# Kernel optimization log

Hardware: AMD Instinct MI355X
Metric: run time of the kernel (lower is better)

The kernel has to match this reference:

```python
import jax, jax.numpy as jnp
import numpy as np

ATTEN_SIZE = 5  # half-window; module-global atten_size in source (0 there is non-functional)
B, S, D_IN, HID, OUT = 8, 2048, 512, 512, 2


def _xavier(key, shape):
    fan_in, fan_out = shape
    std = (2.0 / (fan_in + fan_out)) ** 0.5
    return jax.random.normal(key, shape, dtype=jnp.float32) * std


def setup_inputs() -> dict:
    key = jax.random.key(0)
    ks = jax.random.split(key, 8)
    return {
        "x": jax.random.normal(ks[0], (B, S, D_IN), dtype=jnp.float32),
        "W1": _xavier(ks[1], (D_IN, HID)),
        "b1": jnp.zeros((1, 1, HID), dtype=jnp.float32),
        "Wq": _xavier(ks[2], (HID, HID)),
        "Wk": _xavier(ks[3], (HID, HID)),
        "Wv": _xavier(ks[4], (HID, HID)),
        "W2": _xavier(ks[5], (HID, HID)),
        "b2": jnp.zeros((1, 1, HID), dtype=jnp.float32),
        "Wfc": _xavier(ks[6], (HID, OUT)),
        "bfc": jnp.zeros((OUT,), dtype=jnp.float32),
    }


def reference(x, W1, b1, Wq, Wk, Wv, W2, b2, Wfc, bfc):
    A = ATTEN_SIZE
    Wn = 2 * A + 1
    h = jax.nn.relu(x @ W1 + b1)                      # [B,S,H]
    b, s, hd = h.shape
    padded = jnp.pad(h, ((0, 0), (A, A), (0, 0)))     # [B,S+2A,H]
    # torch pad+roll(k)+stack+slice equals reversed window: x_nei[p, j] = padded[p + 2A - j]
    idx = jnp.arange(s)[:, None] + (2 * A - jnp.arange(Wn))[None, :]  # [S,Wn]
    x_nei = padded[:, idx, :]                         # [B,S,Wn,H]
    q = h @ Wq                                        # [B,S,H]
    k = x_nei @ Wk                                    # [B,S,Wn,H]
    v = x_nei @ Wv                                    # [B,S,Wn,H]
    scale = jnp.asarray(np.sqrt(float(hd)), dtype=h.dtype)
    scores = jnp.einsum('bsh,bswh->bsw', q, k)[:, :, None, :] / scale  # [B,S,1,Wn]
    # Faithful to torch.nn.Softmax(dim=2) on a singleton dim -> all ones
    w = jax.nn.softmax(scores, axis=2)                # [B,S,1,Wn]
    aw = jnp.einsum('bsjw,bswh->bsjh', w, v).reshape(b, s, hd)  # [B,S,H]
    out = jax.nn.relu(aw @ W2 + b2) @ Wfc + bfc       # [B,S,OUT]
    return out, aw
```

## Files before the change

### kernel.cpp

```cpp
#include <hip/hip_runtime.h>
#include <stdint.h>

#define B_   8
#define S_   2048
#define HID_ 512
#define M_   (B_ * S_)
#define AW_  5

typedef __attribute__((ext_vector_type(8))) short bf16x8;
typedef __attribute__((ext_vector_type(4))) float f32x4;
typedef unsigned short u16;

__device__ __forceinline__ u16 f2bf(float f) {
    uint32_t u = __builtin_bit_cast(uint32_t, f);
    u += 0x7FFFu + ((u >> 16) & 1u);
    return (u16)(u >> 16);
}
__device__ __forceinline__ float bf2f(u16 h) {
    uint32_t u = ((uint32_t)h) << 16;
    return __builtin_bit_cast(float, u);
}

__device__ __forceinline__ void gload16(const void* g, void* l) {
    __builtin_amdgcn_global_load_lds(
        (const __attribute__((address_space(1))) void*)(uintptr_t)g,
        (__attribute__((address_space(3))) void*)(uint32_t)(uintptr_t)l,
        16, 0, 0);
}

#define WAITV(n)  asm volatile("s_waitcnt vmcnt(" #n ")" ::: "memory")
#define WAITLG0() asm volatile("s_waitcnt lgkmcnt(0)" ::: "memory")

__global__ __launch_bounds__(256) void prep_w(const float* __restrict__ W1,
                                              const float* __restrict__ Wv,
                                              const float* __restrict__ W2,
                                              u16* __restrict__ W1t,
                                              u16* __restrict__ Wvt,
                                              u16* __restrict__ W2t,
                                              int do_w2) {
    const int wsel = blockIdx.x >> 8;
    if (wsel == 2 && !do_w2) return;
    const float* src = wsel == 0 ? W1 : (wsel == 1 ? Wv : W2);
    u16* dst = wsel == 0 ? W1t : (wsel == 1 ? Wvt : W2t);
    const int t  = blockIdx.x & 255;
    const int n0 = (t & 15) * 32, k0 = (t >> 4) * 32;
    __shared__ float tile[32][33];
    const int tr = threadIdx.x >> 5, tc = threadIdx.x & 31;
#pragma unroll
    for (int p = 0; p < 4; ++p)
        tile[tr + p * 8][tc] = src[(long)(k0 + tr + p * 8) * HID_ + n0 + tc];
    __syncthreads();
#pragma unroll
    for (int p = 0; p < 4; ++p)
        dst[(long)(n0 + tr + p * 8) * HID_ + k0 + tc] = f2bf(tile[tc][tr + p * 8]);
}

__global__ __launch_bounds__(256) void trans_w2(const float* __restrict__ W2,
                                                u16* __restrict__ W2t) {
    __shared__ float tile[32][33];
    const int k0 = blockIdx.y * 32, n0 = blockIdx.x * 32;
    const int tr = threadIdx.x >> 5, tc = threadIdx.x & 31;
#pragma unroll
    for (int p = 0; p < 4; ++p)
        tile[tr + p * 8][tc] = W2[(long)(k0 + tr + p * 8) * HID_ + n0 + tc];
    __syncthreads();
#pragma unroll
    for (int p = 0; p < 4; ++p)
        W2t[(long)(n0 + tr + p * 8) * HID_ + k0 + tc] = f2bf(tile[tc][tr + p * 8]);
}

__global__ __launch_bounds__(256, 2) void gemm1_f32a(const float* __restrict__ A,
                                                     const u16* __restrict__ Bt,
                                                     const float* __restrict__ bias,
                                                     u16* __restrict__ C) {
    __shared__ __attribute__((aligned(16))) u16 As[2][128 * 64];
    __shared__ __attribute__((aligned(16))) u16 Bs[2][128 * 64];

    const int tid = threadIdx.x;
    const int bid = blockIdx.x;
    const int swz = (bid & 7) * 64 + (bid >> 3);
    const int  bn   = (swz & 3) * 128;
    const long brow = (long)(swz >> 2) * 128;

    const int w  = tid >> 6;
    const int l  = tid & 63;
    const int wm = (w >> 1) * 64;
    const int wn = (w & 1) * 64;
    const int lr  = l & 15;
    const int lkb = (l >> 4) * 16;
    const int sw  = (lr & 7) << 4;

    const int r0 = tid >> 2;
    const int c0 = (tid & 3) * 16;
    const int r1 = 64 + r0;
    const float* ga0 = A + (brow + r0) * 512 + c0;
    const float* ga1 = A + (brow + r1) * 512 + c0;
    char* lw = (char*)&As[0][0];
    const int wb00 = r0 * 128 + ((c0 * 2 +  0) ^ ((r0 & 7) << 4));
    const int wb01 = r0 * 128 + ((c0 * 2 + 16) ^ ((r0 & 7) << 4));
    const int wb10 = r1 * 128 + ((c0 * 2 +  0) ^ ((r1 & 7) << 4));
    const int wb11 = r1 * 128 + ((c0 * 2 + 16) ^ ((r1 & 7) << 4));

    int pq[4];
    const u16* srcB[4];
#pragma unroll
    for (int q = 0; q < 4; ++q) {
        const int p   = tid * 16 + q * 4096;
        const int row = p >> 7;
        const int cb  = (p & 127) ^ ((row & 7) << 4);
        pq[q]   = p;
        srcB[q] = Bt + (long)(bn + row) * 512 + (cb >> 1);
    }

    f32x4 acc[4][4];
#pragma unroll
    for (int i = 0; i < 4; ++i)
#pragma unroll
        for (int j = 0; j < 4; ++j) {
            f32x4 z = {0.f, 0.f, 0.f, 0.f};
            acc[i][j] = z;
        }

    float4 ra[4], rb[4];

#define LOADA(k0)                                                        \
    {                                                                    \
        _Pragma("unroll") for (int u = 0; u < 4; ++u) {                  \
            ra[u] = *(const float4*)(ga0 + (k0) + u * 4);                \
            rb[u] = *(const float4*)(ga1 + (k0) + u * 4);                \
        }                                                                \
    }
#define CVTWRITE(buf)                                                    \
    {                                                                    \
        union { u16 u[8]; int4 v; } q0, q1, q2, q3;                      \
        q0.u[0]=f2bf(ra[0].x); q0.u[1]=f2bf(ra[0].y); q0.u[2]=f2bf(ra[0].z); q0.u[3]=f2bf(ra[0].w); \
        q0.u[4]=f2bf(ra[1].x); q0.u[5]=f2bf(ra[1].y); q0.u[6]=f2bf(ra[1].z); q0.u[7]=f2bf(ra[1].w); \
        q1.u[0]=f2bf(ra[2].x); q1.u[1]=f2bf(ra[2].y); q1.u[2]=f2bf(ra[2].z); q1.u[3]=f2bf(ra[2].w); \
        q1.u[4]=f2bf(ra[3].x); q1.u[5]=f2bf(ra[3].y); q1.u[6]=f2bf(ra[3].z); q1.u[7]=f2bf(ra[3].w); \
        q2.u[0]=f2bf(rb[0].x); q2.u[1]=f2bf(rb[0].y); q2.u[2]=f2bf(rb[0].z); q2.u[3]=f2bf(rb[0].w); \
        q2.u[4]=f2bf(rb[1].x); q2.u[5]=f2bf(rb[1].y); q2.u[6]=f2bf(rb[1].z); q2.u[7]=f2bf(rb[1].w); \
        q3.u[0]=f2bf(rb[2].x); q3.u[1]=f2bf(rb[2].y); q3.u[2]=f2bf(rb[2].z); q3.u[3]=f2bf(rb[2].w); \
        q3.u[4]=f2bf(rb[3].x); q3.u[5]=f2bf(rb[3].y); q3.u[6]=f2bf(rb[3].z); q3.u[7]=f2bf(rb[3].w); \
        *(int4*)(lw + (buf) * 16384 + wb00) = q0.v;                      \
        *(int4*)(lw + (buf) * 16384 + wb01) = q1.v;                      \
        *(int4*)(lw + (buf) * 16384 + wb10) = q2.v;                      \
        *(int4*)(lw + (buf) * 16384 + wb11) = q3.v;                      \
    }
#define STAGEB(buf, k0)                                                  \
    {                                                                    \
        _Pragma("unroll") for (int q = 0; q < 4; ++q)                    \
            gload16(srcB[q] + (k0), (char*)&Bs[buf][0] + pq[q]);         \
    }

    LOADA(0);
    STAGEB(0, 0);
    CVTWRITE(0);
    __syncthreads();

    int cur = 0;
    for (int t = 0; t < 8; ++t) {
        if (t < 7) {
            LOADA((t + 1) * 64);
            STAGEB(cur ^ 1, (t + 1) * 64);
        }
#pragma unroll
        for (int kk = 0; kk < 2; ++kk) {
            bf16x8 af[4], bfr[4];
#pragma unroll
            for (int i = 0; i < 4; ++i) {
                const int off = (wm + i * 16 + lr) * 128 + ((kk * 64 + lkb) ^ sw);
                af[i] = *(const bf16x8*)((const char*)&As[cur][0] + off);
            }
#pragma unroll
            for (int j = 0; j < 4; ++j) {
                const int off = (wn + j * 16 + lr) * 128 + ((kk * 64 + lkb) ^ sw);
                bfr[j] = *(const bf16x8*)((const char*)&Bs[cur][0] + off);
            }
#pragma unroll
            for (int i = 0; i < 4; ++i)
#pragma unroll
                for (int j = 0; j < 4; ++j)
                    acc[i][j] = __builtin_amdgcn_mfma_f32_16x16x32_bf16(
                        af[i], bfr[j], acc[i][j], 0, 0, 0);
        }
        if (t < 7) CVTWRITE(cur ^ 1);
        __syncthreads();
        cur ^= 1;
    }
#undef LOADA
#undef CVTWRITE
#undef STAGEB

    float bv[4];
#pragma unroll
    for (int j = 0; j < 4; ++j) bv[j] = bias[bn + wn + j * 16 + lr];
    const int rq = (l >> 4) * 4;
#pragma unroll
    for (int i = 0; i < 4; ++i)
#pragma unroll
        for (int q = 0; q < 4; ++q) {
            const long row = brow + wm + i * 16 + rq + q;
            u16* crow = C + row * 512 + bn + wn + lr;
#pragma unroll
            for (int j = 0; j < 4; ++j)
                crow[j * 16] = f2bf(fmaxf(acc[i][j][q] + bv[j], 0.f));
        }
}

template <int EPI>
__global__ __launch_bounds__(256, 2) void gemm128(const u16* __restrict__ A,
                                                  const u16* __restrict__ Bt,
                                                  const float* __restrict__ b2,
                                                  const float* __restrict__ Wfc,
                                                  u16* __restrict__ C,
                                                  float* __restrict__ partials) {
    __shared__ __attribute__((aligned(16))) u16 As[2][128 * 64];
    __shared__ __attribute__((aligned(16))) u16 Bs[2][128 * 64];

    const int tid = threadIdx.x;
    const int bid = blockIdx.x;
    const int swz = (bid & 7) * 64 + (bid >> 3);
    const int  bn   = (swz & 3) * 128;
    const long brow = (long)(swz >> 2) * 128;

    const int w  = tid >> 6;
    const int l  = tid & 63;
    const int wm = (w >> 1) * 64;
    const int wn = (w & 1) * 64;
    const int lr  = l & 15;
    const int lkb = (l >> 4) * 16;
    const int sw  = (lr & 7) << 4;

    int pq[4];
    const u16* srcA[4];
    const u16* srcB[4];
#pragma unroll
    for (int q = 0; q < 4; ++q) {
        const int p   = tid * 16 + q * 4096;
        const int row = p >> 7;
        const int cb  = (p & 127) ^ ((row & 7) << 4);
        pq[q]   = p;
        srcA[q] = A  + (brow + row) * 512 + (cb >> 1);
        srcB[q] = Bt + (long)(bn + row) * 512 + (cb >> 1);
    }

    f32x4 acc[4][4];
#pragma unroll
    for (int i = 0; i < 4; ++i)
#pragma unroll
        for (int j = 0; j < 4; ++j) {
            f32x4 z = {0.f, 0.f, 0.f, 0.f};
            acc[i][j] = z;
        }

#define STAGE(buf, k0)                                                   \
    {                                                                    \
        _Pragma("unroll") for (int q = 0; q < 4; ++q) {                  \
            gload16(srcA[q] + (k0), (char*)&As[buf][0] + pq[q]);         \
            gload16(srcB[q] + (k0), (char*)&Bs[buf][0] + pq[q]);         \
        }                                                                \
    }

    int cur = 0;
    STAGE(0, 0);
    __syncthreads();

    for (int t = 0; t < 8; ++t) {
        if (t < 7) STAGE(cur ^ 1, (t + 1) * 64);
#pragma unroll
        for (int kk = 0; kk < 2; ++kk) {
            bf16x8 af[4], bfr[4];
#pragma unroll
            for (int i = 0; i < 4; ++i) {
                const int off = (wm + i * 16 + lr) * 128 + ((kk * 64 + lkb) ^ sw);
                af[i] = *(const bf16x8*)((const char*)&As[cur][0] + off);
            }
#pragma unroll
            for (int j = 0; j < 4; ++j) {
                const int off = (wn + j * 16 + lr) * 128 + ((kk * 64 + lkb) ^ sw);
                bfr[j] = *(const bf16x8*)((const char*)&Bs[cur][0] + off);
            }
#pragma unroll
            for (int i = 0; i < 4; ++i)
#pragma unroll
                for (int j = 0; j < 4; ++j)
                    acc[i][j] = __builtin_amdgcn_mfma_f32_16x16x32_bf16(
                        af[i], bfr[j], acc[i][j], 0, 0, 0);
        }
        __syncthreads();
        cur ^= 1;
    }
#undef STAGE

    const int rq = (l >> 4) * 4;
    if (EPI == 0) {
#pragma unroll
        for (int i = 0; i < 4; ++i)
#pragma unroll
            for (int q = 0; q < 4; ++q) {
                const long row = brow + wm + i * 16 + rq + q;
                u16* crow = C + row * 512 + bn + wn + lr;
#pragma unroll
                for (int j = 0; j < 4; ++j)
                    crow[j * 16] = f2bf(acc[i][j][q]);
            }
    } else {
        float bvv[4], w0v[4], w1v[4];
#pragma unroll
        for (int j = 0; j < 4; ++j) {
            const int col = bn + wn + j * 16 + lr;
            bvv[j] = b2[col];
            w0v[j] = Wfc[2 * col];
            w1v[j] = Wfc[2 * col + 1];
        }
        const int slot = (bn >> 7) * 2 + (wn >> 6);
#pragma unroll
        for (int i = 0; i < 4; ++i)
#pragma unroll
            for (int q = 0; q < 4; ++q) {
                float s0 = 0.f, s1 = 0.f;
#pragma unroll
                for (int j = 0; j < 4; ++j) {
                    const float v = fmaxf(acc[i][j][q] + bvv[j], 0.f);
                    s0 += v * w0v[j];
                    s1 += v * w1v[j];
                }
#pragma unroll
                for (int m = 1; m < 16; m <<= 1) {
                    s0 += __shfl_xor(s0, m);
                    s1 += __shfl_xor(s1, m);
                }
                if (lr == 0) {
                    const long row = brow + wm + i * 16 + rq + q;
                    float* pp = partials + ((long)slot * M_ + row) * 2;
                    pp[0] = s0;
                    pp[1] = s1;
                }
            }
    }
}

__global__ __launch_bounds__(512, 2) void gemm2_ws(const u16* __restrict__ A,
                                                   const u16* __restrict__ Bt,
                                                   u16* __restrict__ awb,
                                                   float* __restrict__ awf) {
    __shared__ __attribute__((aligned(16))) u16 As[3][288 * 64];
    __shared__ __attribute__((aligned(16))) u16 Bs[3][128 * 64];

    const int tid = threadIdx.x;
    const int bid = blockIdx.x;
    const int swz = (bid & 7) * 32 + (bid >> 3);
    const int  bn   = (swz & 3) * 128;
    const long brow = (long)(swz >> 2) * 256;

    const int w  = tid >> 6;
    const int l  = tid & 63;
    const int wm = (w >> 2) * 144;
    const int wn = (w & 3) * 32;
    const int lr  = l & 15;
    const int lkb = (l >> 4) * 16;
    const int sw  = (lr & 7) << 4;
    const bool loww = (tid < 256);

    int pa[5];
    const u16* srcA[5];
#pragma unroll
    for (int q = 0; q < 4; ++q) {
        const int p   = tid * 16 + q * 8192;
        const int row = p >> 7;
        const int cb  = (p & 127) ^ ((row & 7) << 4);
        long R = brow - 16 + row;
        R = R < 0 ? 0 : (R > M_ - 1 ? M_ - 1 : R);
        pa[q]   = p;
        srcA[q] = A + R * 512 + (cb >> 1);
    }
    pa[4] = 0; srcA[4] = A;
    if (loww) {
        const int p   = 32768 + tid * 16;
        const int row = p >> 7;
        const int cb  = (p & 127) ^ ((row & 7) << 4);
        long R = brow - 16 + row;
        R = R < 0 ? 0 : (R > M_ - 1 ? M_ - 1 : R);
        pa[4]   = p;
        srcA[4] = A + R * 512 + (cb >> 1);
    }
    int pb[2];
    const u16* srcB[2];
#pragma unroll
    for (int q = 0; q < 2; ++q) {
        const int p   = tid * 16 + q * 8192;
        const int row = p >> 7;
        const int cb  = (p & 127) ^ ((row & 7) << 4);
        pb[q]   = p;
        srcB[q] = Bt + (long)(bn + row) * 512 + (cb >> 1);
    }

    f32x4 acc[9][2];
#pragma unroll
    for (int i = 0; i < 9; ++i)
#pragma unroll
        for (int j = 0; j < 2; ++j) {
            f32x4 z = {0.f, 0.f, 0.f, 0.f};
            acc[i][j] = z;
        }

#define STG(buf, k0)                                                     \
    {                                                                    \
        gload16(srcA[0] + (k0), (char*)&As[buf][0] + pa[0]);             \
        gload16(srcA[1] + (k0), (char*)&As[buf][0] + pa[1]);             \
        gload16(srcA[2] + (k0), (char*)&As[buf][0] + pa[2]);             \
        gload16(srcA[3] + (k0), (char*)&As[buf][0] + pa[3]);             \
        if (loww) gload16(srcA[4] + (k0), (char*)&As[buf][0] + pa[4]);   \
        gload16(srcB[0] + (k0), (char*)&Bs[buf][0] + pb[0]);             \
        gload16(srcB[1] + (k0), (char*)&Bs[buf][0] + pb[1]);             \
    }
#define WAITP()                                                          \
    do {                                                                 \
        if (loww) { WAITV(7); } else { WAITV(6); }                       \
    } while (0)

    STG(0, 0);
    STG(1, 64);
    WAITP();
    __builtin_amdgcn_s_barrier();

#pragma unroll
    for (int t = 0; t < 8; ++t) {
        if (t < 6) {
            const int nb = (t + 2) % 3;
            if (nb == 0)      STG(0, (t + 2) * 64)
            else if (nb == 1) STG(1, (t + 2) * 64)
            else              STG(2, (t + 2) * 64)
        }

        const int cbuf = t % 3;
        const char* ab = cbuf == 0 ? (const char*)&As[0][0]
                       : cbuf == 1 ? (const char*)&As[1][0] : (const char*)&As[2][0];
        const char* bb = cbuf == 0 ? (const char*)&Bs[0][0]
                       : cbuf == 1 ? (const char*)&Bs[1][0] : (const char*)&Bs[2][0];

        __builtin_amdgcn_s_setprio(1);
#pragma unroll
        for (int kk = 0; kk < 2; ++kk) {
            bf16x8 af[9], bfr[2];
#pragma unroll
            for (int j = 0; j < 2; ++j) {
                const int off = (wn + j * 16 + lr) * 128 + ((kk * 64 + lkb) ^ sw);
                bfr[j] = *(const bf16x8*)(bb + off);
            }
#pragma unroll
            for (int i = 0; i < 9; ++i) {
                const int off = (wm + i * 16 + lr) * 128 + ((kk * 64 + lkb) ^ sw);
                af[i] = *(const bf16x8*)(ab + off);
            }
#pragma unroll
            for (int i = 0; i < 9; ++i)
#pragma unroll
                for (int j = 0; j < 2; ++j)
                    acc[i][j] = __builtin_amdgcn_mfma_f32_16x16x32_bf16(
                        af[i], bfr[j], acc[i][j], 0, 0, 0);
        }
        __builtin_amdgcn_s_setprio(0);

        if (t < 7) {
            WAITLG0();
            __builtin_amdgcn_sched_barrier(0);
            if (t < 6) { WAITP(); } else { WAITV(0); }
            __builtin_amdgcn_s_barrier();
        }
    }
#undef STG
#undef WAITP

    __syncthreads();
    u16* gl = &As[0][0];

    const int rq4 = (l >> 4) * 4;
#pragma unroll
    for (int i = 0; i < 9; ++i)
#pragma unroll
        for (int j = 0; j < 2; ++j)
#pragma unroll
            for (int q = 0; q < 4; ++q) {
                const int row = wm + i * 16 + rq4 + q;
                const int col = wn + j * 16 + lr;
                gl[row * 128 + col] = f2bf(acc[i][j][q]);
            }
    __syncthreads();

    for (int rr = 0; rr < 32; ++rr) {
        const int  rloc = w * 32 + rr;
        const long R    = brow + rloc;
        const int  s    = (int)(R & (S_ - 1));
        float a0 = 0.f, a1 = 0.f;
#pragma unroll
        for (int d = -AW_; d <= AW_; ++d) {
            if ((unsigned)(s + d) < (unsigned)S_) {
                const uint32_t v =
                    *(const uint32_t*)&gl[(rloc + 16 + d) * 128 + 2 * l];
                a0 += bf2f((u16)(v & 0xffffu));
                a1 += bf2f((u16)(v >> 16));
            }
        }
        const uint32_t pk = (uint32_t)f2bf(a0) | ((uint32_t)f2bf(a1) << 16);
        *(uint32_t*)&awb[R * 512 + bn + 2 * l] = pk;
        float2 o; o.x = a0; o.y = a1;
        *(float2*)&awf[R * 512 + bn + 2 * l] = o;
    }
}

__global__ __launch_bounds__(256) void winsum_f(const u16* __restrict__ g,
                                                u16* __restrict__ awb,
                                                float* __restrict__ awf) {
    const long idx = (long)blockIdx.x * 256 + threadIdx.x;
    const int  c8  = (int)(idx & 63);
    const long bs  = idx >> 6;
    const int  s   = (int)(bs & (S_ - 1));

    float acc[8] = {};
#pragma unroll
    for (int d = -AW_; d <= AW_; ++d) {
        const int ss = s + d;
        if (0 <= ss && ss < S_) {
            const int4 v = *(const int4*)&g[(bs + d) * HID_ + c8 * 8];
            const u16* u = (const u16*)&v;
#pragma unroll
            for (int e = 0; e < 8; ++e) acc[e] += bf2f(u[e]);
        }
    }
    union { u16 u[8]; int4 v; } r;
#pragma unroll
    for (int e = 0; e < 8; ++e) r.u[e] = f2bf(acc[e]);
    *(int4*)&awb[bs * HID_ + c8 * 8] = r.v;
    float4 o0 = {acc[0], acc[1], acc[2], acc[3]};
    float4 o1 = {acc[4], acc[5], acc[6], acc[7]};
    *(float4*)&awf[bs * HID_ + c8 * 8]     = o0;
    *(float4*)&awf[bs * HID_ + c8 * 8 + 4] = o1;
}

__global__ __launch_bounds__(256) void fc_reduce(const float* __restrict__ partials,
                                                 const float* __restrict__ bfc,
                                                 float* __restrict__ out) {
    const int row = blockIdx.x * 256 + threadIdx.x;
    float s0 = bfc[0], s1 = bfc[1];
#pragma unroll
    for (int p = 0; p < 8; ++p) {
        s0 += partials[((long)p * M_ + row) * 2 + 0];
        s1 += partials[((long)p * M_ + row) * 2 + 1];
    }
    out[row * 2 + 0] = s0;
    out[row * 2 + 1] = s1;
}

extern "C" void kernel_launch(void* const* d_in, const int* in_sizes, int n_in,
                              void* d_out, int out_size, void* d_ws, size_t ws_size,
                              hipStream_t stream) {
    const float* x   = (const float*)d_in[0];
    const float* W1  = (const float*)d_in[1];
    const float* b1  = (const float*)d_in[2];
    const float* Wv  = (const float*)d_in[5];
    const float* W2  = (const float*)d_in[6];
    const float* b2  = (const float*)d_in[7];
    const float* Wfc = (const float*)d_in[8];
    const float* bfc = (const float*)d_in[9];

    float* out_part = (float*)d_out;
    float* aw_f32   = (float*)d_out + (long)M_ * 2;

    unsigned char* ws = (unsigned char*)d_ws;

    const bool big = ws_size >= ((size_t)35 << 20);

    if (big) {
        u16* h    = (u16*)ws;
        u16* awb  = (u16*)(ws + (16l << 20));
        u16* W1t  = (u16*)(ws + (32l << 20));
        u16* Wvt  = W1t + 262144;
        u16* W2t  = Wvt + 262144;
        float* partials = (float*)(ws + (33l << 20) + (1l << 19));

        prep_w<<<768, 256, 0, stream>>>(W1, Wv, W2, W1t, Wvt, W2t, 1);
        gemm1_f32a<<<512, 256, 0, stream>>>(x, W1t, b1, h);
        gemm2_ws<<<256, 512, 0, stream>>>(h, Wvt, awb, aw_f32);
        gemm128<1><<<512, 256, 0, stream>>>(awb, W2t, b2, Wfc, nullptr, partials);
        fc_reduce<<<64, 256, 0, stream>>>(partials, bfc, out_part);
    } else {
        u16* W1t = (u16*)aw_f32;
        u16* Wvt = W1t + 262144;
        u16* h   = (u16*)ws;
        u16* g   = (u16*)ws + 8388608;
        u16* awb = h;
        u16* W2t = g;
        float* partials = (float*)(ws + (17l << 20));

        prep_w<<<768, 256, 0, stream>>>(W1, Wv, W2, W1t, Wvt, W2t, 0);
        gemm1_f32a<<<512, 256, 0, stream>>>(x, W1t, b1, h);
        gemm128<0><<<512, 256, 0, stream>>>(h, Wvt, nullptr, nullptr, g, nullptr);
        winsum_f<<<4096, 256, 0, stream>>>(g, awb, aw_f32);
        trans_w2<<<dim3(16, 16), 256, 0, stream>>>(W2, W2t);
        gemm128<1><<<512, 256, 0, stream>>>(awb, W2t, b2, Wfc, nullptr, partials);
        fc_reduce<<<64, 256, 0, stream>>>(partials, bfc, out_part);
    }
}
```

Baseline: 75.43 us.

## Interleave global prefetch with MFMA in gemm2_ws and add 256-row final GEMM

The windowed gemm2_ws kernel now splits its A-fragment loads and MFMA work into two halves per k-substep, issuing the next-stage global-to-LDS copies between them so memory traffic overlaps compute instead of sitting in front of it. A new gemm4_256 kernel with 512 threads and 256x128 tiles replaces gemm128<1> for the W2/ReLU/Wfc projection on the large-workspace path, using the same interleaved prefetch. Its partial sums go to 16 slots, so fc_reduce now takes a slot count. This adds reduction traffic and LDS pressure from larger tiles in exchange for fewer blocks and better overlap.

Measured after the change: 80.82 us. +7.1%, slower.

```diff
diff --git a/kernel.cpp b/kernel.cpp
--- a/kernel.cpp
+++ b/kernel.cpp
@@ -426,39 +426,65 @@
 
 #pragma unroll
     for (int t = 0; t < 8; ++t) {
-        if (t < 6) {
-            const int nb = (t + 2) % 3;
-            if (nb == 0)      STG(0, (t + 2) * 64)
-            else if (nb == 1) STG(1, (t + 2) * 64)
-            else              STG(2, (t + 2) * 64)
-        }
-
         const int cbuf = t % 3;
         const char* ab = cbuf == 0 ? (const char*)&As[0][0]
                        : cbuf == 1 ? (const char*)&As[1][0] : (const char*)&As[2][0];
         const char* bb = cbuf == 0 ? (const char*)&Bs[0][0]
                        : cbuf == 1 ? (const char*)&Bs[1][0] : (const char*)&Bs[2][0];
+        const int nb = (t + 2) % 3;
+        char* an = nb == 0 ? (char*)&As[0][0]
+                 : nb == 1 ? (char*)&As[1][0] : (char*)&As[2][0];
+        char* bs2 = nb == 0 ? (char*)&Bs[0][0]
+                  : nb == 1 ? (char*)&Bs[1][0] : (char*)&Bs[2][0];
+        const int k2 = (t + 2) * 64;
+        const bool stg = (t < 6);
 
         __builtin_amdgcn_s_setprio(1);
 #pragma unroll
         for (int kk = 0; kk < 2; ++kk) {
-            bf16x8 af[9], bfr[2];
+            bf16x8 bfr[2], af0[5], af1[4];
 #pragma unroll
             for (int j = 0; j < 2; ++j) {
                 const int off = (wn + j * 16 + lr) * 128 + ((kk * 64 + lkb) ^ sw);
                 bfr[j] = *(const bf16x8*)(bb + off);
             }
 #pragma unroll
-            for (int i = 0; i < 9; ++i) {
+            for (int i = 0; i < 5; ++i) {
                 const int off = (wm + i * 16 + lr) * 128 + ((kk * 64 + lkb) ^ sw);
-                af[i] = *(const bf16x8*)(ab + off);
-            }
-#pragma unroll
-            for (int i = 0; i < 9; ++i)
+                af0[i] = *(const bf16x8*)(ab + off);
+            }
+            if (stg && kk == 0) {
+                gload16(srcA[0] + k2, an + pa[0]);
+                gload16(srcA[1] + k2, an + pa[1]);
+            }
+            if (stg && kk == 1) {
+                gload16(srcB[0] + k2, bs2 + pb[0]);
+                gload16(srcB[1] + k2, bs2 + pb[1]);
+            }
+            __builtin_amdgcn_sched_barrier(0);
+#pragma unroll
+            for (int i = 0; i < 5; ++i)
 #pragma unroll
                 for (int j = 0; j < 2; ++j)
                     acc[i][j] = __builtin_amdgcn_mfma_f32_16x16x32_bf16(
-                        af[i], bfr[j], acc[i][j], 0, 0, 0);
+                        af0[i], bfr[j], acc[i][j], 0, 0, 0);
+#pragma unroll
+            for (int i = 0; i < 4; ++i) {
+                const int off = (wm + (5 + i) * 16 + lr) * 128 + ((kk * 64 + lkb) ^ sw);
+                af1[i] = *(const bf16x8*)(ab + off);
+            }
+            if (stg && kk == 0) {
+                gload16(srcA[2] + k2, an + pa[2]);
+                gload16(srcA[3] + k2, an + pa[3]);
+                if (loww) gload16(srcA[4] + k2, an + pa[4]);
+            }
+            __builtin_amdgcn_sched_barrier(0);
+#pragma unroll
+            for (int i = 0; i < 4; ++i)
+#pragma unroll
+                for (int j = 0; j < 2; ++j)
+                    acc[5 + i][j] = __builtin_amdgcn_mfma_f32_16x16x32_bf16(
+                        af1[i], bfr[j], acc[5 + i][j], 0, 0, 0);
         }
         __builtin_amdgcn_s_setprio(0);
 
@@ -507,6 +533,179 @@
         float2 o; o.x = a0; o.y = a1;
         *(float2*)&awf[R * 512 + bn + 2 * l] = o;
     }
+}
+
+__global__ __launch_bounds__(512, 2) void gemm4_256(const u16* __restrict__ A,
+                                                    const u16* __restrict__ Bt,
+                                                    const float* __restrict__ b2,
+                                                    const float* __restrict__ Wfc,
+                                                    float* __restrict__ partials) {
+    __shared__ __attribute__((aligned(16))) u16 As[3][256 * 64];
+    __shared__ __attribute__((aligned(16))) u16 Bs[3][128 * 64];
+
+    const int tid = threadIdx.x;
+    const int bid = blockIdx.x;
+    const int swz = (bid & 7) * 32 + (bid >> 3);
+    const int  bn   = (swz & 3) * 128;
+    const long brow = (long)(swz >> 2) * 256;
+
+    const int w  = tid >> 6;
+    const int l  = tid & 63;
+    const int wm = (w >> 2) * 128;
+    const int wn = (w & 3) * 32;
+    const int lr  = l & 15;
+    const int lkb = (l >> 4) * 16;
+    const int sw  = (lr & 7) << 4;
+
+    int pa[4], pb[2];
+    const u16* srcA[4];
+    const u16* srcB[2];
+#pragma unroll
+    for (int q = 0; q < 4; ++q) {
+        const int p   = tid * 16 + q * 8192;
+        const int row = p >> 7;
+        const int cb  = (p & 127) ^ ((row & 7) << 4);
+        pa[q]   = p;
+        srcA[q] = A + (brow + row) * 512 + (cb >> 1);
+    }
+#pragma unroll
+    for (int q = 0; q < 2; ++q) {
+        const int p   = tid * 16 + q * 8192;
+        const int row = p >> 7;
+        const int cb  = (p & 127) ^ ((row & 7) << 4);
+        pb[q]   = p;
+        srcB[q] = Bt + (long)(bn + row) * 512 + (cb >> 1);
+    }
+
+    f32x4 acc[8][2];
+#pragma unroll
+    for (int i = 0; i < 8; ++i)
+#pragma unroll
+        for (int j = 0; j < 2; ++j) {
+            f32x4 z = {0.f, 0.f, 0.f, 0.f};
+            acc[i][j] = z;
+        }
+
+#define STG(buf, k0)                                                     \
+    {                                                                    \
+        gload16(srcA[0] + (k0), (char*)&As[buf][0] + pa[0]);             \
+        gload16(srcA[1] + (k0), (char*)&As[buf][0] + pa[1]);             \
+        gload16(srcA[2] + (k0), (char*)&As[buf][0] + pa[2]);             \
+        gload16(srcA[3] + (k0), (char*)&As[buf][0] + pa[3]);             \
+        gload16(srcB[0] + (k0), (char*)&Bs[buf][0] + pb[0]);             \
+        gload16(srcB[1] + (k0), (char*)&Bs[buf][0] + pb[1]);             \
+    }
+
+    STG(0, 0);
+    STG(1, 64);
+    WAITV(6);
+    __builtin_amdgcn_s_barrier();
+
+#pragma unroll
+    for (int t = 0; t < 8; ++t) {
+        const int cbuf = t % 3;
+        const char* ab = cbuf == 0 ? (const char*)&As[0][0]
+                       : cbuf == 1 ? (const char*)&As[1][0] : (const char*)&As[2][0];
+        const char* bb = cbuf == 0 ? (const char*)&Bs[0][0]
+                       : cbuf == 1 ? (const char*)&Bs[1][0] : (const char*)&Bs[2][0];
+        const int nb = (t + 2) % 3;
+        char* an = nb == 0 ? (char*)&As[0][0]
+                 : nb == 1 ? (char*)&As[1][0] : (char*)&As[2][0];
+        char* bs2 = nb == 0 ? (char*)&Bs[0][0]
+                  : nb == 1 ? (char*)&Bs[1][0] : (char*)&Bs[2][0];
+        const int k2 = (t + 2) * 64;
+        const bool stg = (t < 6);
+
+        __builtin_amdgcn_s_setprio(1);
+#pragma unroll
+        for (int kk = 0; kk < 2; ++kk) {
+            bf16x8 bfr[2], af0[4], af1[4];
+#pragma unroll
+            for (int j = 0; j < 2; ++j) {
+                const int off = (wn + j * 16 + lr) * 128 + ((kk * 64 + lkb) ^ sw);
+                bfr[j] = *(const bf16x8*)(bb + off);
+            }
+#pragma unroll
+            for (int i = 0; i < 4; ++i) {
+                const int off = (wm + i * 16 + lr) * 128 + ((kk * 64 + lkb) ^ sw);
+                af0[i] = *(const bf16x8*)(ab + off);
+            }
+            if (stg && kk == 0) {
+                gload16(srcA[0] + k2, an + pa[0]);
+                gload16(srcA[1] + k2, an + pa[1]);
+            }
+            if (stg && kk == 1) {
+                gload16(srcB[0] + k2, bs2 + pb[0]);
+                gload16(srcB[1] + k2, bs2 + pb[1]);
+            }
+            __builtin_amdgcn_sched_barrier(0);
+#pragma unroll
+            for (int i = 0; i < 4; ++i)
+#pragma unroll
+                for (int j = 0; j < 2; ++j)
+                    acc[i][j] = __builtin_amdgcn_mfma_f32_16x16x32_bf16(
+                        af0[i], bfr[j], acc[i][j], 0, 0, 0);
+#pragma unroll
+            for (int i = 0; i < 4; ++i) {
+                const int off = (wm + (4 + i) * 16 + lr) * 128 + ((kk * 64 + lkb) ^ sw);
+                af1[i] = *(const bf16x8*)(ab + off);
+            }
+            if (stg && kk == 0) {
+                gload16(srcA[2] + k2, an + pa[2]);
+                gload16(srcA[3] + k2, an + pa[3]);
+            }
+            __builtin_amdgcn_sched_barrier(0);
+#pragma unroll
+            for (int i = 0; i < 4; ++i)
+#pragma unroll
+                for (int j = 0; j < 2; ++j)
+                    acc[4 + i][j] = __builtin_amdgcn_mfma_f32_16x16x32_bf16(
+                        af1[i], bfr[j], acc[4 + i][j], 0, 0, 0);
+        }
+        __builtin_amdgcn_s_setprio(0);
+
+        if (t < 7) {
+            WAITLG0();
+            __builtin_amdgcn_sched_barrier(0);
+            if (t < 6) { WAITV(6); } else { WAITV(0); }
+            __builtin_amdgcn_s_barrier();
+        }
+    }
+#undef STG
+
+    float bvv[2], w0v[2], w1v[2];
+#pragma unroll
+    for (int j = 0; j < 2; ++j) {
+        const int col = bn + wn + j * 16 + lr;
+        bvv[j] = b2[col];
+        w0v[j] = Wfc[2 * col];
+        w1v[j] = Wfc[2 * col + 1];
+    }
+    const int rq = (l >> 4) * 4;
+    const int slot = (bn >> 7) * 4 + (w & 3);
+#pragma unroll
+    for (int i = 0; i < 8; ++i)
+#pragma unroll
+        for (int q = 0; q < 4; ++q) {
+            float s0 = 0.f, s1 = 0.f;
+#pragma unroll
+            for (int j = 0; j < 2; ++j) {
+                const float v = fmaxf(acc[i][j][q] + bvv[j], 0.f);
+                s0 += v * w0v[j];
+                s1 += v * w1v[j];
+            }
+#pragma unroll
+            for (int m = 1; m < 16; m <<= 1) {
+                s0 += __shfl_xor(s0, m);
+                s1 += __shfl_xor(s1, m);
+            }
+            if (lr == 0) {
+                const long row = brow + wm + i * 16 + rq + q;
+                float* pp = partials + ((long)slot * M_ + row) * 2;
+                pp[0] = s0;
+                pp[1] = s1;
+            }
+        }
 }
 
 __global__ __launch_bounds__(256) void winsum_f(const u16* __restrict__ g,
@@ -540,11 +739,11 @@
 
 __global__ __launch_bounds__(256) void fc_reduce(const float* __restrict__ partials,
                                                  const float* __restrict__ bfc,
-                                                 float* __restrict__ out) {
+                                                 float* __restrict__ out,
+                                                 int nslot) {
     const int row = blockIdx.x * 256 + threadIdx.x;
     float s0 = bfc[0], s1 = bfc[1];
-#pragma unroll
-    for (int p = 0; p < 8; ++p) {
+    for (int p = 0; p < nslot; ++p) {
         s0 += partials[((long)p * M_ + row) * 2 + 0];
         s1 += partials[((long)p * M_ + row) * 2 + 1];
     }
@@ -582,8 +781,8 @@
         prep_w<<<768, 256, 0, stream>>>(W1, Wv, W2, W1t, Wvt, W2t, 1);
         gemm1_f32a<<<512, 256, 0, stream>>>(x, W1t, b1, h);
         gemm2_ws<<<256, 512, 0, stream>>>(h, Wvt, awb, aw_f32);
-        gemm128<1><<<512, 256, 0, stream>>>(awb, W2t, b2, Wfc, nullptr, partials);
-        fc_reduce<<<64, 256, 0, stream>>>(partials, bfc, out_part);
+        gemm4_256<<<256, 512, 0, stream>>>(awb, W2t, b2, Wfc, partials);
+        fc_reduce<<<64, 256, 0, stream>>>(partials, bfc, out_part, 16);
     } else {
         u16* W1t = (u16*)aw_f32;
         u16* Wvt = W1t + 262144;
@@ -599,6 +798,6 @@
         winsum_f<<<4096, 256, 0, stream>>>(g, awb, aw_f32);
         trans_w2<<<dim3(16, 16), 256, 0, stream>>>(W2, W2t);
         gemm128<1><<<512, 256, 0, stream>>>(awb, W2t, b2, Wfc, nullptr, partials);
-        fc_reduce<<<64, 256, 0, stream>>>(partials, bfc, out_part);
-    }
-}
+        fc_reduce<<<64, 256, 0, stream>>>(partials, bfc, out_part, 8);
+    }
+}
```
